# Optimization experiments

Hardware: AMD Instinct MI355X
Metric: run time of the kernel (lower is better)

## Reference

```python
import jax, jax.numpy as jnp
import numpy as np

B, S, H, STEPS = 4096, 169, 64, 24  # batch, input seq (window 168 + covariate row), hidden, rollout steps


def _lstm(xseq, Wih, Whh, bih, bhh, h0, c0):
    """PyTorch-style single-layer LSTM. xseq: [B,T,D] -> ([B,T,H], hT, cT). Gate order i,f,g,o."""
    xg = jnp.einsum('btd,gd->btg', xseq, Wih) + (bih + bhh)  # precompute input proj [B,T,4H]

    def step(carry, xg_t):
        h, c = carry
        g = xg_t + h @ Whh.T
        i, f, gg, o = jnp.split(g, 4, axis=-1)
        c = jax.nn.sigmoid(f) * c + jax.nn.sigmoid(i) * jnp.tanh(gg)
        h = jax.nn.sigmoid(o) * jnp.tanh(c)
        return (h, c), h

    (hT, cT), hs = jax.lax.scan(step, (h0, c0), jnp.swapaxes(xg, 0, 1))
    return jnp.swapaxes(hs, 0, 1), hT, cT


def reference(x, Wih1, Whh1, bih1, bhh1, Wih2, Whh2, bih2, bhh2, fc1_w, fc1_b, fc2_w, fc2_b):
    win, d = x[:, :-1, :], x[:, -1, :]  # [B,168,1], [B,1]
    z = jnp.zeros((x.shape[0], H), x.dtype)

    def outer(win, _):
        h1s, h1, c1 = _lstm(win, Wih1, Whh1, bih1, bhh1, z, z)
        h1s = jax.nn.relu(h1s)
        # lstm2 is seeded with lstm1's final (h, c) state, as in the torch code
        h2s, _, _ = _lstm(h1s, Wih2, Whh2, bih2, bhh2, h1, c1)
        feat = jnp.concatenate([jax.nn.relu(h2s[:, -1, :]), d], axis=1)  # [B,65]
        out = (feat @ fc1_w.T + fc1_b) @ fc2_w.T + fc2_b  # [B,1] (no relu between fc1/fc2)
        win = jnp.concatenate([win[:, 1:, :], out[:, :, None]], axis=1)  # slide window
        return win, out[:, 0]

    _, outs = jax.lax.scan(outer, win, None, length=STEPS)  # outs: [24,B]
    return jnp.swapaxes(outs, 0, 1)  # [B,24]


def setup_inputs() -> dict:
    key = jax.random.key(0)
    ks = jax.random.split(key, 14)
    bnd = 1.0 / np.sqrt(H)

    def u(k, shape):
        return jax.random.uniform(k, shape, jnp.float32, -bnd, bnd)

    return {
        'x': jax.random.normal(ks[0], (B, S, 1), jnp.float32),
        'Wih1': u(ks[1], (4 * H, 1)),
        'Whh1': u(ks[2], (4 * H, H)),
        'bih1': u(ks[3], (4 * H,)),
        'bhh1': u(ks[4], (4 * H,)),
        'Wih2': u(ks[5], (4 * H, H)),
        'Whh2': u(ks[6], (4 * H, H)),
        'bih2': u(ks[7], (4 * H,)),
        'bhh2': u(ks[8], (4 * H,)),
        'fc1_w': u(ks[9], (64, 65)),
        'fc1_b': u(ks[10], (64,)),
        'fc2_w': u(ks[11], (1, 64)),
        'fc2_b': u(ks[12], (1,)),
    }
```

## Files before the change

### kernel.cpp

```cpp
#include <hip/hip_runtime.h>
#include <stdint.h>

#define NB 16
#define WIN 168
#define NSTEPS 24
#define NBLK (4096/NB)
#define NT 512

typedef __attribute__((ext_vector_type(8))) short bf16x8;
typedef __attribute__((ext_vector_type(4))) float f32x4;

#if __has_builtin(__builtin_amdgcn_rcpf)
#define RCPF(x) __builtin_amdgcn_rcpf(x)
#else
#define RCPF(x) (1.0f / (x))
#endif
#if __has_builtin(__builtin_amdgcn_exp2f)
#define EXP2F(x) __builtin_amdgcn_exp2f(x)
#else
#define EXP2F(x) __expf((x) * 0.6931471805599453f)
#endif

__device__ __forceinline__ float sigm(float x){
  return RCPF(1.0f + EXP2F(x * -1.4426950408889634f));
}
__device__ __forceinline__ float sigtanh(float a, float b){
  float A = EXP2F(a * -1.4426950408889634f);
  float B = EXP2F(fabsf(b) * -2.8853900817779268f);
  float t = (1.0f - B) * RCPF((1.0f + A) * (1.0f + B));
  return __builtin_copysignf(t, b);
}

__device__ __forceinline__ uint32_t bf_rn(float f){
  uint32_t u = __builtin_bit_cast(uint32_t, f);
  return (u + 0x7FFFu + ((u >> 16) & 1u)) >> 16;
}
__device__ __forceinline__ float bf_f(uint32_t s){
  return __builtin_bit_cast(float, s << 16);
}
__device__ __forceinline__ void split_t(float f, uint32_t& hi, uint32_t& lo){
  uint32_t u = __builtin_bit_cast(uint32_t, f);
  hi = u >> 16;
  lo = bf_rn(f - bf_f(hi));
}
__device__ __forceinline__ void split_s(float f, short& hi, short& lo){
  uint32_t h = bf_rn(f);
  hi = (short)h;
  lo = (short)bf_rn(f - bf_f(h));
}
__device__ __forceinline__ uint32_t cvtpk2(float a, float b){
  uint32_t r;
  asm("v_cvt_pk_bf16_f32 %0, %1, %2" : "=v"(r) : "v"(a), "v"(b));
  return r;
}
__device__ __forceinline__ float hi_even(uint32_t p){
  return __builtin_bit_cast(float, p << 16);
}
__device__ __forceinline__ float hi_odd(uint32_t p){
  return __builtin_bit_cast(float, p & 0xFFFF0000u);
}
__device__ __forceinline__ f32x4 mfma16(bf16x8 a, bf16x8 b, f32x4 c){
  return __builtin_amdgcn_mfma_f32_16x16x32_bf16(a, b, c, 0, 0, 0);
}

#define FROW 136
#define FBLK 544
#define FB(buf,hl,kt) ((((buf)*2 + (hl))*2 + (kt)) * FBLK)
#define BUF_INTS (2*FBLK)

__global__ __launch_bounds__(NT, 2) void lstm_fused_kernel(
  const float* __restrict__ x,    const float* __restrict__ Wih1, const float* __restrict__ Whh1,
  const float* __restrict__ bih1, const float* __restrict__ bhh1,
  const float* __restrict__ Wih2, const float* __restrict__ Whh2,
  const float* __restrict__ bih2, const float* __restrict__ bhh2,
  const float* __restrict__ fc1w, const float* __restrict__ fc1b,
  const float* __restrict__ fc2w, const float* __restrict__ fc2b,
  float* __restrict__ out, short* __restrict__ hist)
{
  __shared__ __align__(16) short aS[2*2*2*FBLK];
  __shared__ __align__(16) short bS[2*2*2*FBLK];
  __shared__ float win_s[WIN][NB];
  __shared__ float Hlast[NB][68];
  __shared__ float fc1w_s[64*68];
  __shared__ float dval_s[NB];

  const int tid = threadIdx.x;
  const int w   = tid >> 6;
  const int ln  = tid & 63;
  const int q   = ln >> 4;
  const int n   = ln & 15;
  const int bg0 = blockIdx.x * NB;
  const int rdo = q*FROW + n*8;
  const int ro  = q*128 + n*8;
  const int ktw = w >> 2;
  const int wrw = (w&3)*FROW + n*8 + 2*q;
  const int hwo = ktw*512 + (w&3)*128 + n*8 + 2*q;
  short* __restrict__ hblk = hist + (size_t)blockIdx.x * WIN * 2048;

  for (int i = tid; i < WIN*NB; i += NT){ int t = i >> 4, b = i & 15; win_s[t][b] = x[(bg0 + b)*169 + t]; }
  for (int i = tid; i < 64*65; i += NT){ int j = i / 65, k = i % 65; fc1w_s[j*68 + k] = fc1w[i]; }
  if (tid < NB) dval_s[tid] = x[(bg0 + tid)*169 + 168];

  const float fc1b_r = fc1b[ln];
  const float fc2w_r = fc2w[ln];
  const float fc2b_r = fc2b[0];

  auto fc_head = [&](int s){
    float o2[2];
    #pragma unroll
    for (int bi = 0; bi < 2; bi++){
      const int b = 2*w + bi;
      float a1 = fc1b_r;
      #pragma unroll
      for (int k4 = 0; k4 < 16; k4++){
        const float* wp = &fc1w_s[ln*68 + k4*4];
        const float* hp = &Hlast[b][k4*4];
        a1 += wp[0]*hp[0] + wp[1]*hp[1] + wp[2]*hp[2] + wp[3]*hp[3];
      }
      a1 += dval_s[b] * fc1w_s[ln*68 + 64];
      float v = a1 * fc2w_r;
      #pragma unroll
      for (int off = 32; off > 0; off >>= 1) v += __shfl_xor(v, off);
      o2[bi] = v + fc2b_r;
    }
    if (ln == 0){
      #pragma unroll
      for (int bi = 0; bi < 2; bi++){
        const int b = 2*w + bi;
        out[(bg0 + b)*24 + s] = o2[bi];
        win_s[s % WIN][b] = o2[bi];
      }
    }
  };

  bf16x8 A1hi[2][2], A1lo[2][2], Ain1[2];
  bf16x8 A2hi[2][4], A2lo[2][4];
  f32x4 b1c[2], b2c[2];
  #pragma unroll
  for (int tu = 0; tu < 2; tu++){
    const int jA = 64*(n&3) + 8*w + 2*(n>>2) + tu;
    #pragma unroll
    for (int kt = 0; kt < 2; kt++){
      const float* pw = Whh1 + jA*64 + kt*32 + q*8;
      #pragma unroll
      for (int jj = 0; jj < 8; jj++){ short h,l; split_s(pw[jj], h, l); A1hi[tu][kt][jj] = h; A1lo[tu][kt][jj] = l; }
    }
    bf16x8 ain = {0,0,0,0,0,0,0,0};
    if (q == 0){ short wh, wl; split_s(Wih1[jA], wh, wl); ain[0] = wh; ain[1] = wh; ain[2] = wl; }
    Ain1[tu] = ain;
    #pragma unroll
    for (int kt = 0; kt < 4; kt++){
      const float* pw = (kt < 2 ? (Wih2 + jA*64 + kt*32) : (Whh2 + jA*64 + (kt-2)*32)) + q*8;
      #pragma unroll
      for (int jj = 0; jj < 8; jj++){ short h,l; split_s(pw[jj], h, l); A2hi[tu][kt][jj] = h; A2lo[tu][kt][jj] = l; }
    }
    const int U = 8*w + 2*q + tu;
    #pragma unroll
    for (int r = 0; r < 4; r++){
      b1c[tu][r] = bih1[64*r + U] + bhh1[64*r + U];
      b2c[tu][r] = bih2[64*r + U] + bhh2[64*r + U];
    }
  }

  float c1[2], c1sav[2], c2[2];
  bf16x8 hA0, lA0, hA1, lA1, hB0, lB0, hB1, lB1;

  auto loadA = [&](int t){
    const short* Hp = hblk + (size_t)t * 2048;
    hA0 = *(const bf16x8*)&Hp[ro];
    lA0 = *(const bf16x8*)&Hp[1024 + ro];
    hA1 = *(const bf16x8*)&Hp[512 + ro];
    lA1 = *(const bf16x8*)&Hp[1536 + ro];
  };
  auto loadB = [&](int t){
    const short* Hp = hblk + (size_t)t * 2048;
    hB0 = *(const bf16x8*)&Hp[ro];
    lB0 = *(const bf16x8*)&Hp[1024 + ro];
    hB1 = *(const bf16x8*)&Hp[512 + ro];
    lB1 = *(const bf16x8*)&Hp[1536 + ro];
  };

  auto lstm1 = [&](int rb, int wb, int slot, int t, bool first){
    bf16x8 bin = {0,0,0,0,0,0,0,0};
    { float xv = win_s[slot][n];
      uint32_t xp = cvtpk2(xv, xv);
      float rx = xv - hi_even(xp);
      uint32_t xq = cvtpk2(rx, rx);
      if (q == 0){ bin[0] = (short)xp; bin[1] = (short)xq; bin[2] = (short)xp; } }
    f32x4 acc[2];
    if (first){
      #pragma unroll
      for (int tu = 0; tu < 2; tu++) acc[tu] = mfma16(Ain1[tu], bin, b1c[tu]);
    } else {
      bf16x8 Bh0 = *(const bf16x8*)&aS[FB(rb,0,0)+rdo];
      bf16x8 Bl0 = *(const bf16x8*)&aS[FB(rb,1,0)+rdo];
      bf16x8 Bh1 = *(const bf16x8*)&aS[FB(rb,0,1)+rdo];
      bf16x8 Bl1 = *(const bf16x8*)&aS[FB(rb,1,1)+rdo];
      #pragma unroll
      for (int tu = 0; tu < 2; tu++){
        f32x4 a = b1c[tu];
        a = mfma16(A1hi[tu][0], Bh0, a);
        a = mfma16(A1hi[tu][0], Bl0, a);
        a = mfma16(A1lo[tu][0], Bh0, a);
        a = mfma16(A1hi[tu][1], Bh1, a);
        a = mfma16(A1hi[tu][1], Bl1, a);
        a = mfma16(A1lo[tu][1], Bh1, a);
        a = mfma16(Ain1[tu], bin, a);
        acc[tu] = a;
      }
    }
    float hn[2];
    #pragma unroll
    for (int tu = 0; tu < 2; tu++){
      float cn = __builtin_fmaf(sigm(acc[tu][1]), c1[tu], sigtanh(acc[tu][0], acc[tu][2]));
      c1[tu] = cn;
      hn[tu] = sigtanh(acc[tu][3], cn);
    }
    uint32_t p  = cvtpk2(hn[0], hn[1]);
    float r0 = hn[0] - hi_even(p), r1 = hn[1] - hi_odd(p);
    uint32_t ql = cvtpk2(r0, r1);
    *(uint32_t*)&aS[FB(wb,0,ktw)+wrw] = p;
    *(uint32_t*)&aS[FB(wb,1,ktw)+wrw] = ql;
    uint32_t m = (hn[0] > 0.0f ? 0x0000FFFFu : 0u) | (hn[1] > 0.0f ? 0xFFFF0000u : 0u);
    short* Hp = hblk + (size_t)t * 2048;
    *(uint32_t*)&Hp[hwo]        = p  & m;
    *(uint32_t*)&Hp[1024 + hwo] = ql & m;
  };

  auto lstm2 = [&](bf16x8 h0, bf16x8 l0, bf16x8 h1, bf16x8 l1,
                   const short* Sr, int rb, short* Sw, int wb, bool last){
    bf16x8 Sh0 = *(const bf16x8*)&Sr[FB(rb,0,0)+rdo];
    bf16x8 Sl0 = *(const bf16x8*)&Sr[FB(rb,1,0)+rdo];
    bf16x8 Sh1 = *(const bf16x8*)&Sr[FB(rb,0,1)+rdo];
    bf16x8 Sl1 = *(const bf16x8*)&Sr[FB(rb,1,1)+rdo];
    f32x4 acc[2];
    #pragma unroll
    for (int tu = 0; tu < 2; tu++){
      f32x4 a = b2c[tu];
      a = mfma16(A2hi[tu][0], h0, a);
      a = mfma16(A2hi[tu][0], l0, a);
      a = mfma16(A2lo[tu][0], h0, a);
      a = mfma16(A2hi[tu][1], h1, a);
      a = mfma16(A2hi[tu][1], l1, a);
      a = mfma16(A2lo[tu][1], h1, a);
      a = mfma16(A2hi[tu][2], Sh0, a);
      a = mfma16(A2hi[tu][2], Sl0, a);
      a = mfma16(A2lo[tu][2], Sh0, a);
      a = mfma16(A2hi[tu][3], Sh1, a);
      a = mfma16(A2hi[tu][3], Sl1, a);
      a = mfma16(A2lo[tu][3], Sh1, a);
      acc[tu] = a;
    }
    float hn[2];
    #pragma unroll
    for (int tu = 0; tu < 2; tu++){
      float cn = __builtin_fmaf(sigm(acc[tu][1]), c2[tu], sigtanh(acc[tu][0], acc[tu][2]));
      c2[tu] = cn;
      hn[tu] = sigtanh(acc[tu][3], cn);
    }
    if (!last){
      uint32_t p  = cvtpk2(hn[0], hn[1]);
      float r0 = hn[0] - hi_even(p), r1 = hn[1] - hi_odd(p);
      uint32_t ql = cvtpk2(r0, r1);
      *(uint32_t*)&Sw[FB(wb,0,ktw)+wrw] = p;
      *(uint32_t*)&Sw[FB(wb,1,ktw)+wrw] = ql;
    } else {
      const int U0 = 8*w + 2*q;
      Hlast[n][U0]     = fmaxf(hn[0], 0.0f);
      Hlast[n][U0 + 1] = fmaxf(hn[1], 0.0f);
    }
  };

  c1[0] = 0.0f; c1[1] = 0.0f;
  __syncthreads();
  lstm1(0, 1, 0, 0, true);
  for (int t = 1; t < WIN-1; t += 2){
    __syncthreads();
    lstm1(1, 0, t, t, false);
    __syncthreads();
    lstm1(0, 1, t+1, t+1, false);
  }
  __syncthreads();
  lstm1(1, 0, WIN-1, WIN-1, false);
  c1sav[0] = c1[0]; c1sav[1] = c1[1];

  for (int sg = 1; sg < NSTEPS; sg++){
    c2[0] = c1sav[0]; c2[1] = c1sav[1];
    c1[0] = 0.0f;     c1[1] = 0.0f;
    loadA(0); loadB(1);
    int slot = sg;
    __syncthreads();
    lstm1(0, 1, slot, 0, true); slot++;
    lstm2(hA0, lA0, hA1, lA1, aS, 0, bS, 1, false);
    for (int t = 1; t < WIN-1; t += 2){
      __syncthreads();
      loadA(t + 1);
      lstm1(1, 0, slot, t, false); slot++; if (slot == WIN) slot = 0;
      lstm2(hB0, lB0, hB1, lB1, bS, 1, bS, 0, false);
      __syncthreads();
      loadB(t + 2);
      lstm1(0, 1, slot, t+1, false); slot++; if (slot == WIN) slot = 0;
      lstm2(hA0, lA0, hA1, lA1, bS, 0, bS, 1, false);
    }
    __syncthreads();
    lstm2(hB0, lB0, hB1, lB1, bS, 1, bS, 0, true);
    __syncthreads();
    fc_head(sg - 1);
    __syncthreads();
    lstm1(1, 0, slot, WIN-1, false);
    c1sav[0] = c1[0]; c1sav[1] = c1[1];
  }

  {
    c2[0] = c1sav[0]; c2[1] = c1sav[1];
    loadA(0); loadB(1);
    __syncthreads();
    lstm2(hA0, lA0, hA1, lA1, aS, 0, bS, 1, false);
    for (int t = 1; t < WIN-1; t += 2){
      __syncthreads();
      loadA(t + 1);
      lstm2(hB0, lB0, hB1, lB1, bS, 1, bS, 0, false);
      __syncthreads();
      loadB(t + 2);
      lstm2(hA0, lA0, hA1, lA1, bS, 0, bS, 1, false);
    }
    __syncthreads();
    lstm2(hB0, lB0, hB1, lB1, bS, 1, bS, 0, true);
    __syncthreads();
    fc_head(NSTEPS - 1);
  }
}

__global__ __launch_bounds__(256, 1) void lstm_fallback_kernel(
  const float* __restrict__ x,    const float* __restrict__ Wih1, const float* __restrict__ Whh1,
  const float* __restrict__ bih1, const float* __restrict__ bhh1,
  const float* __restrict__ Wih2, const float* __restrict__ Whh2,
  const float* __restrict__ bih2, const float* __restrict__ bhh2,
  const float* __restrict__ fc1w, const float* __restrict__ fc1b,
  const float* __restrict__ fc2w, const float* __restrict__ fc2b,
  float* __restrict__ out)
{
  __shared__ __align__(16) short aS[2*2*2*FBLK];
  __shared__ __align__(16) short r1f[2*2*2*FBLK];
  __shared__ __align__(16) short rlf[2*2*2*FBLK];
  __shared__ float win_s[WIN][NB];
  __shared__ float Hlast[NB][68];
  __shared__ float fc1w_s[64*68];
  __shared__ float dval_s[NB];

  const int tid = threadIdx.x;
  const int wv  = tid >> 6;
  const int ln  = tid & 63;
  const int q   = ln >> 4;
  const int n   = ln & 15;
  const int bg0 = blockIdx.x * NB;
  const int u0  = 16*wv + 4*q;
  const int kt_  = u0 >> 5;
  const int q2_  = (u0 >> 3) & 3;
  const int jj0_ = u0 & 7;
  const int rdo  = q*FROW + n*8;
  const int wro  = q2_*FROW + n*8 + jj0_;

  for (int i = tid; i < WIN*NB; i += 256){ int t = i >> 4, b = i & 15; win_s[t][b] = x[(bg0 + b)*169 + t]; }
  for (int i = tid; i < 64*65; i += 256){ int j = i / 65, k = i % 65; fc1w_s[j*68 + k] = fc1w[i]; }
  if (tid < NB) dval_s[tid] = x[(bg0 + tid)*169 + 168];

  const float fc1b_r = fc1b[ln];
  const float fc2w_r = fc2w[ln];
  const float fc2b_r = fc2b[0];

  bf16x8 A1hi[4][2], A1lo[4][2], Ain1[4];
  bf16x8 A2hi[4][4], A2lo[4][4];
  f32x4 b1c[4], b2c[4];
  #pragma unroll
  for (int e = 0; e < 4; e++){
    const int ja = 64*e + 16*wv + n;
    #pragma unroll
    for (int kt = 0; kt < 2; kt++){
      const float* pw = Whh1 + ja*64 + kt*32 + q*8;
      #pragma unroll
      for (int jj = 0; jj < 8; jj++){ short h,l; split_s(pw[jj], h, l); A1hi[e][kt][jj] = h; A1lo[e][kt][jj] = l; }
    }
    #pragma unroll
    for (int kt = 0; kt < 4; kt++){
      const float* pw = (kt < 2 ? (Wih2 + ja*64 + kt*32) : (Whh2 + ja*64 + (kt-2)*32)) + q*8;
      #pragma unroll
      for (int jj = 0; jj < 8; jj++){ short h,l; split_s(pw[jj], h, l); A2hi[e][kt][jj] = h; A2lo[e][kt][jj] = l; }
    }
    bf16x8 ain = {0,0,0,0,0,0,0,0};
    if (q == 0){ short wh, wl; split_s(Wih1[ja], wh, wl); ain[0] = wh; ain[1] = wh; ain[2] = wl; }
    Ain1[e] = ain;
    const int jc = 64*e + u0;
    #pragma unroll
    for (int r = 0; r < 4; r++){
      b1c[e][r] = bih1[jc+r] + bhh1[jc+r];
      b2c[e][r] = bih2[jc+r] + bhh2[jc+r];
    }
  }

  float c1[4], c2[4], c1r[4];

  auto lstm1_step = [&](short* S, float* cst, int rb, int wb, int slot, bool relu_out){
    bf16x8 Bh0 = *(const bf16x8*)&S[FB(rb,0,0)+rdo];
    bf16x8 Bl0 = *(const bf16x8*)&S[FB(rb,1,0)+rdo];
    bf16x8 Bh1 = *(const bf16x8*)&S[FB(rb,0,1)+rdo];
    bf16x8 Bl1 = *(const bf16x8*)&S[FB(rb,1,1)+rdo];
    bf16x8 bin = {0,0,0,0,0,0,0,0};
    { float xv = win_s[slot][n]; uint32_t xh, xl; split_t(xv, xh, xl);
      if (q == 0){ bin[0] = (short)xh; bin[1] = (short)xl; bin[2] = (short)xh; } }
    f32x4 acc[4];
    #pragma unroll
    for (int e = 0; e < 4; e++){
      f32x4 a = b1c[e];
      a = mfma16(A1hi[e][0], Bh0, a);
      a = mfma16(A1hi[e][0], Bl0, a);
      a = mfma16(A1lo[e][0], Bh0, a);
      a = mfma16(A1hi[e][1], Bh1, a);
      a = mfma16(A1hi[e][1], Bl1, a);
      a = mfma16(A1lo[e][1], Bh1, a);
      a = mfma16(Ain1[e], bin, a);
      acc[e] = a;
    }
    float hn[4];
    #pragma unroll
    for (int r = 0; r < 4; r++){
      float cn = __builtin_fmaf(sigm(acc[1][r]), cst[r], sigtanh(acc[0][r], acc[2][r]));
      cst[r] = cn;
      hn[r] = sigtanh(acc[3][r], cn);
    }
    uint32_t ph[4], pl[4];
    #pragma unroll
    for (int r = 0; r < 4; r++) split_t(hn[r], ph[r], pl[r]);
    *(uint2*)&S[FB(wb,0,kt_)+wro] = make_uint2(ph[0] | (ph[1]<<16), ph[2] | (ph[3]<<16));
    *(uint2*)&S[FB(wb,1,kt_)+wro] = make_uint2(pl[0] | (pl[1]<<16), pl[2] | (pl[3]<<16));
    if (relu_out){
      uint32_t sh[4], sl[4];
      #pragma unroll
      for (int r = 0; r < 4; r++){ bool pos = hn[r] > 0.0f; sh[r] = pos ? ph[r] : 0u; sl[r] = pos ? pl[r] : 0u; }
      *(uint2*)&rlf[FB(rb,0,kt_)+wro] = make_uint2(sh[0] | (sh[1]<<16), sh[2] | (sh[3]<<16));
      *(uint2*)&rlf[FB(rb,1,kt_)+wro] = make_uint2(sl[0] | (sl[1]<<16), sl[2] | (sl[3]<<16));
    }
  };

  auto lstm2_core = [&](bf16x8 L1h0, bf16x8 L1l0, bf16x8 L1h1, bf16x8 L1l1,
                        int rbuf, int wbuf, bool last){
    bf16x8 L2h0 = *(const bf16x8*)&aS[FB(rbuf,0,0)+rdo];
    bf16x8 L2l0 = *(const bf16x8*)&aS[FB(rbuf,1,0)+rdo];
    bf16x8 L2h1 = *(const bf16x8*)&aS[FB(rbuf,0,1)+rdo];
    bf16x8 L2l1 = *(const bf16x8*)&aS[FB(rbuf,1,1)+rdo];
    f32x4 acc[4];
    #pragma unroll
    for (int e = 0; e < 4; e++){
      f32x4 a = b2c[e];
      a = mfma16(A2hi[e][0], L1h0, a);
      a = mfma16(A2hi[e][0], L1l0, a);
      a = mfma16(A2lo[e][0], L1h0, a);
      a = mfma16(A2hi[e][1], L1h1, a);
      a = mfma16(A2hi[e][1], L1l1, a);
      a = mfma16(A2lo[e][1], L1h1, a);
      a = mfma16(A2hi[e][2], L2h0, a);
      a = mfma16(A2hi[e][2], L2l0, a);
      a = mfma16(A2lo[e][2], L2h0, a);
      a = mfma16(A2hi[e][3], L2h1, a);
      a = mfma16(A2hi[e][3], L2l1, a);
      a = mfma16(A2lo[e][3], L2h1, a);
      acc[e] = a;
    }
    float hn[4];
    #pragma unroll
    for (int r = 0; r < 4; r++){
      float cn = __builtin_fmaf(sigm(acc[1][r]), c2[r], sigtanh(acc[0][r], acc[2][r]));
      c2[r] = cn;
      hn[r] = sigtanh(acc[3][r], cn);
    }
    if (!last){
      uint32_t ph[4], pl[4];
      #pragma unroll
      for (int r = 0; r < 4; r++) split_t(hn[r], ph[r], pl[r]);
      *(uint2*)&aS[FB(wbuf,0,kt_)+wro] = make_uint2(ph[0] | (ph[1]<<16), ph[2] | (ph[3]<<16));
      *(uint2*)&aS[FB(wbuf,1,kt_)+wro] = make_uint2(pl[0] | (pl[1]<<16), pl[2] | (pl[3]<<16));
    } else {
      #pragma unroll
      for (int r = 0; r < 4; r++) Hlast[n][u0 + r] = fmaxf(hn[r], 0.0f);
    }
  };

  for (int s = 0; s < NSTEPS; s++){
    { int* p = (int*)&aS[0];
      for (int i = tid; i < BUF_INTS; i += 256) p[i] = 0; }
    #pragma unroll
    for (int r = 0; r < 4; r++) c1[r] = 0.0f;
    int slot = s;
    for (int t = 0; t < WIN; t++){
      __syncthreads();
      lstm1_step(aS, c1, t & 1, (t & 1) ^ 1, slot, false);
      slot++; if (slot == WIN) slot = 0;
    }
    #pragma unroll
    for (int r = 0; r < 4; r++){ c2[r] = c1[r]; c1r[r] = 0.0f; }
    { int* p = (int*)&r1f[0];
      for (int i = tid; i < BUF_INTS; i += 256) p[i] = 0; }
    slot = s;
    __syncthreads();
    lstm1_step(r1f, c1r, 0, 1, slot, true);
    slot++;
    for (int i = 1; i < WIN; i++){
      __syncthreads();
      const int rb = i & 1, wb = rb ^ 1;
      lstm1_step(r1f, c1r, rb, wb, slot, true);
      bf16x8 L1h0 = *(const bf16x8*)&rlf[FB(wb,0,0)+rdo];
      bf16x8 L1l0 = *(const bf16x8*)&rlf[FB(wb,1,0)+rdo];
      bf16x8 L1h1 = *(const bf16x8*)&rlf[FB(wb,0,1)+rdo];
      bf16x8 L1l1 = *(const bf16x8*)&rlf[FB(wb,1,1)+rdo];
      lstm2_core(L1h0, L1l0, L1h1, L1l1, wb, rb, false);
      slot++; if (slot == WIN) slot = 0;
    }
    __syncthreads();
    {
      const int rb = (WIN - 1) & 1;
      bf16x8 L1h0 = *(const bf16x8*)&rlf[FB(rb,0,0)+rdo];
      bf16x8 L1l0 = *(const bf16x8*)&rlf[FB(rb,1,0)+rdo];
      bf16x8 L1h1 = *(const bf16x8*)&rlf[FB(rb,0,1)+rdo];
      bf16x8 L1l1 = *(const bf16x8*)&rlf[FB(rb,1,1)+rdo];
      lstm2_core(L1h0, L1l0, L1h1, L1l1, rb, 0, true);
    }
    __syncthreads();
    {
      float o4[4];
      #pragma unroll
      for (int bi = 0; bi < 4; bi++){
        const int b = 4*wv + bi;
        float a1 = fc1b_r;
        #pragma unroll
        for (int k4 = 0; k4 < 16; k4++){
          const float* wp = &fc1w_s[ln*68 + k4*4];
          const float* hp = &Hlast[b][k4*4];
          a1 += wp[0]*hp[0] + wp[1]*hp[1] + wp[2]*hp[2] + wp[3]*hp[3];
        }
        a1 += dval_s[b] * fc1w_s[ln*68 + 64];
        float v = a1 * fc2w_r;
        #pragma unroll
        for (int off = 32; off > 0; off >>= 1) v += __shfl_xor(v, off);
        o4[bi] = v + fc2b_r;
      }
      if (ln == 0){
        #pragma unroll
        for (int bi = 0; bi < 4; bi++){
          const int b = 4*wv + bi;
          out[(bg0 + b)*24 + s] = o4[bi];
          win_s[s % WIN][b] = o4[bi];
        }
      }
    }
  }
}

extern "C" void kernel_launch(void* const* d_in, const int* in_sizes, int n_in,
                              void* d_out, int out_size, void* d_ws, size_t ws_size,
                              hipStream_t stream) {
  (void)in_sizes; (void)n_in; (void)out_size;
  const size_t need = (size_t)NBLK * WIN * 2048 * sizeof(short);
  if (ws_size >= need){
    lstm_fused_kernel<<<dim3(NBLK), dim3(NT), 0, stream>>>(
        (const float*)d_in[0], (const float*)d_in[1], (const float*)d_in[2],
        (const float*)d_in[3], (const float*)d_in[4], (const float*)d_in[5],
        (const float*)d_in[6], (const float*)d_in[7], (const float*)d_in[8],
        (const float*)d_in[9], (const float*)d_in[10], (const float*)d_in[11],
        (const float*)d_in[12], (float*)d_out, (short*)d_ws);
  } else {
    lstm_fallback_kernel<<<dim3(NBLK), dim3(256), 0, stream>>>(
        (const float*)d_in[0], (const float*)d_in[1], (const float*)d_in[2],
        (const float*)d_in[3], (const float*)d_in[4], (const float*)d_in[5],
        (const float*)d_in[6], (const float*)d_in[7], (const float*)d_in[8],
        (const float*)d_in[9], (const float*)d_in[10], (const float*)d_in[11],
        (const float*)d_in[12], (float*)d_out);
  }
}
```

Before: 5.010 ms.

## Split LSTM layers across specialized wave groups with doubled block size

Doubles the block to 1024 threads. The first 8 waves run only the layer-1 recurrence and the other 8 run only the layer-2 recurrence, so both layers advance concurrently in separate waves. The two groups stay in lockstep through matched barrier counts, and the layer-1 final cell state is handed to layer 2 through a new shared-memory array. The aim is a shorter serial chain per timestep and fewer live weight registers per wave. The cost is a more fragile barrier protocol and a launch-bounds occupancy hint of 4 blocks of 1024 threads, which may squeeze the per-thread register budget and cause spills.

```diff
diff --git a/kernel.cpp b/kernel.cpp
--- a/kernel.cpp
+++ b/kernel.cpp
@@ -5,7 +5,7 @@
 #define WIN 168
 #define NSTEPS 24
 #define NBLK (4096/NB)
-#define NT 512
+#define NT 1024
 
 typedef __attribute__((ext_vector_type(8))) short bf16x8;
 typedef __attribute__((ext_vector_type(4))) float f32x4;
@@ -68,7 +68,7 @@
 #define FB(buf,hl,kt) ((((buf)*2 + (hl))*2 + (kt)) * FBLK)
 #define BUF_INTS (2*FBLK)
 
-__global__ __launch_bounds__(NT, 2) void lstm_fused_kernel(
+__global__ __launch_bounds__(NT, 4) void lstm_fused_kernel(
   const float* __restrict__ x,    const float* __restrict__ Wih1, const float* __restrict__ Whh1,
   const float* __restrict__ bih1, const float* __restrict__ bhh1,
   const float* __restrict__ Wih2, const float* __restrict__ Whh2,
@@ -79,13 +79,16 @@
 {
   __shared__ __align__(16) short aS[2*2*2*FBLK];
   __shared__ __align__(16) short bS[2*2*2*FBLK];
+  __shared__ float cS[64][16];
   __shared__ float win_s[WIN][NB];
   __shared__ float Hlast[NB][68];
   __shared__ float fc1w_s[64*68];
   __shared__ float dval_s[NB];
 
   const int tid = threadIdx.x;
-  const int w   = tid >> 6;
+  const int w16 = tid >> 6;
+  const int w   = w16 & 7;
+  const bool isA = (w16 < 8);
   const int ln  = tid & 63;
   const int q   = ln >> 4;
   const int n   = ln & 15;
@@ -106,228 +109,261 @@
   const float fc2b_r = fc2b[0];
 
   auto fc_head = [&](int s){
-    float o2[2];
-    #pragma unroll
-    for (int bi = 0; bi < 2; bi++){
-      const int b = 2*w + bi;
-      float a1 = fc1b_r;
-      #pragma unroll
-      for (int k4 = 0; k4 < 16; k4++){
-        const float* wp = &fc1w_s[ln*68 + k4*4];
-        const float* hp = &Hlast[b][k4*4];
-        a1 += wp[0]*hp[0] + wp[1]*hp[1] + wp[2]*hp[2] + wp[3]*hp[3];
-      }
-      a1 += dval_s[b] * fc1w_s[ln*68 + 64];
-      float v = a1 * fc2w_r;
-      #pragma unroll
-      for (int off = 32; off > 0; off >>= 1) v += __shfl_xor(v, off);
-      o2[bi] = v + fc2b_r;
-    }
+    const int b = w16;
+    float a1 = fc1b_r;
+    #pragma unroll
+    for (int k4 = 0; k4 < 16; k4++){
+      const float* wp = &fc1w_s[ln*68 + k4*4];
+      const float* hp = &Hlast[b][k4*4];
+      a1 += wp[0]*hp[0] + wp[1]*hp[1] + wp[2]*hp[2] + wp[3]*hp[3];
+    }
+    a1 += dval_s[b] * fc1w_s[ln*68 + 64];
+    float v = a1 * fc2w_r;
+    #pragma unroll
+    for (int off = 32; off > 0; off >>= 1) v += __shfl_xor(v, off);
     if (ln == 0){
-      #pragma unroll
-      for (int bi = 0; bi < 2; bi++){
-        const int b = 2*w + bi;
-        out[(bg0 + b)*24 + s] = o2[bi];
-        win_s[s % WIN][b] = o2[bi];
-      }
+      float o = v + fc2b_r;
+      out[(bg0 + b)*24 + s] = o;
+      win_s[s % WIN][b] = o;
     }
   };
 
-  bf16x8 A1hi[2][2], A1lo[2][2], Ain1[2];
-  bf16x8 A2hi[2][4], A2lo[2][4];
-  f32x4 b1c[2], b2c[2];
-  #pragma unroll
-  for (int tu = 0; tu < 2; tu++){
-    const int jA = 64*(n&3) + 8*w + 2*(n>>2) + tu;
-    #pragma unroll
-    for (int kt = 0; kt < 2; kt++){
-      const float* pw = Whh1 + jA*64 + kt*32 + q*8;
-      #pragma unroll
-      for (int jj = 0; jj < 8; jj++){ short h,l; split_s(pw[jj], h, l); A1hi[tu][kt][jj] = h; A1lo[tu][kt][jj] = l; }
-    }
-    bf16x8 ain = {0,0,0,0,0,0,0,0};
-    if (q == 0){ short wh, wl; split_s(Wih1[jA], wh, wl); ain[0] = wh; ain[1] = wh; ain[2] = wl; }
-    Ain1[tu] = ain;
-    #pragma unroll
-    for (int kt = 0; kt < 4; kt++){
-      const float* pw = (kt < 2 ? (Wih2 + jA*64 + kt*32) : (Whh2 + jA*64 + (kt-2)*32)) + q*8;
-      #pragma unroll
-      for (int jj = 0; jj < 8; jj++){ short h,l; split_s(pw[jj], h, l); A2hi[tu][kt][jj] = h; A2lo[tu][kt][jj] = l; }
-    }
-    const int U = 8*w + 2*q + tu;
-    #pragma unroll
-    for (int r = 0; r < 4; r++){
-      b1c[tu][r] = bih1[64*r + U] + bhh1[64*r + U];
-      b2c[tu][r] = bih2[64*r + U] + bhh2[64*r + U];
-    }
-  }
-
-  float c1[2], c1sav[2], c2[2];
-  bf16x8 hA0, lA0, hA1, lA1, hB0, lB0, hB1, lB1;
-
-  auto loadA = [&](int t){
-    const short* Hp = hblk + (size_t)t * 2048;
-    hA0 = *(const bf16x8*)&Hp[ro];
-    lA0 = *(const bf16x8*)&Hp[1024 + ro];
-    hA1 = *(const bf16x8*)&Hp[512 + ro];
-    lA1 = *(const bf16x8*)&Hp[1536 + ro];
-  };
-  auto loadB = [&](int t){
-    const short* Hp = hblk + (size_t)t * 2048;
-    hB0 = *(const bf16x8*)&Hp[ro];
-    lB0 = *(const bf16x8*)&Hp[1024 + ro];
-    hB1 = *(const bf16x8*)&Hp[512 + ro];
-    lB1 = *(const bf16x8*)&Hp[1536 + ro];
-  };
-
-  auto lstm1 = [&](int rb, int wb, int slot, int t, bool first){
-    bf16x8 bin = {0,0,0,0,0,0,0,0};
-    { float xv = win_s[slot][n];
-      uint32_t xp = cvtpk2(xv, xv);
-      float rx = xv - hi_even(xp);
-      uint32_t xq = cvtpk2(rx, rx);
-      if (q == 0){ bin[0] = (short)xp; bin[1] = (short)xq; bin[2] = (short)xp; } }
-    f32x4 acc[2];
-    if (first){
-      #pragma unroll
-      for (int tu = 0; tu < 2; tu++) acc[tu] = mfma16(Ain1[tu], bin, b1c[tu]);
-    } else {
-      bf16x8 Bh0 = *(const bf16x8*)&aS[FB(rb,0,0)+rdo];
-      bf16x8 Bl0 = *(const bf16x8*)&aS[FB(rb,1,0)+rdo];
-      bf16x8 Bh1 = *(const bf16x8*)&aS[FB(rb,0,1)+rdo];
-      bf16x8 Bl1 = *(const bf16x8*)&aS[FB(rb,1,1)+rdo];
+  if (isA){
+    bf16x8 A1hi[2][2], A1lo[2][2], Ain1[2];
+    f32x4 b1c[2];
+    #pragma unroll
+    for (int tu = 0; tu < 2; tu++){
+      const int jA = 64*(n&3) + 8*w + 2*(n>>2) + tu;
+      #pragma unroll
+      for (int kt = 0; kt < 2; kt++){
+        const float* pw = Whh1 + jA*64 + kt*32 + q*8;
+        #pragma unroll
+        for (int jj = 0; jj < 8; jj++){ short h,l; split_s(pw[jj], h, l); A1hi[tu][kt][jj] = h; A1lo[tu][kt][jj] = l; }
+      }
+      bf16x8 ain = {0,0,0,0,0,0,0,0};
+      if (q == 0){ short wh, wl; split_s(Wih1[jA], wh, wl); ain[0] = wh; ain[1] = wh; ain[2] = wl; }
+      Ain1[tu] = ain;
+      const int U = 8*w + 2*q + tu;
+      #pragma unroll
+      for (int r = 0; r < 4; r++) b1c[tu][r] = bih1[64*r + U] + bhh1[64*r + U];
+    }
+    float c1[2];
+
+    auto lstm1 = [&](int rb, int wb, int slot, int t, bool first){
+      bf16x8 bin = {0,0,0,0,0,0,0,0};
+      { float xv = win_s[slot][n];
+        uint32_t xp = cvtpk2(xv, xv);
+        float rx = xv - hi_even(xp);
+        uint32_t xq = cvtpk2(rx, rx);
+        if (q == 0){ bin[0] = (short)xp; bin[1] = (short)xq; bin[2] = (short)xp; } }
+      f32x4 acc[2];
+      if (first){
+        #pragma unroll
+        for (int tu = 0; tu < 2; tu++) acc[tu] = mfma16(Ain1[tu], bin, b1c[tu]);
+      } else {
+        bf16x8 Bh0 = *(const bf16x8*)&aS[FB(rb,0,0)+rdo];
+        bf16x8 Bl0 = *(const bf16x8*)&aS[FB(rb,1,0)+rdo];
+        bf16x8 Bh1 = *(const bf16x8*)&aS[FB(rb,0,1)+rdo];
+        bf16x8 Bl1 = *(const bf16x8*)&aS[FB(rb,1,1)+rdo];
+        #pragma unroll
+        for (int tu = 0; tu < 2; tu++){
+          f32x4 a = b1c[tu];
+          a = mfma16(A1hi[tu][0], Bh0, a);
+          a = mfma16(A1hi[tu][0], Bl0, a);
+          a = mfma16(A1lo[tu][0], Bh0, a);
+          a = mfma16(A1hi[tu][1], Bh1, a);
+          a = mfma16(A1hi[tu][1], Bl1, a);
+          a = mfma16(A1lo[tu][1], Bh1, a);
+          a = mfma16(Ain1[tu], bin, a);
+          acc[tu] = a;
+        }
+      }
+      float hn[2];
       #pragma unroll
       for (int tu = 0; tu < 2; tu++){
-        f32x4 a = b1c[tu];
-        a = mfma16(A1hi[tu][0], Bh0, a);
-        a = mfma16(A1hi[tu][0], Bl0, a);
-        a = mfma16(A1lo[tu][0], Bh0, a);
-        a = mfma16(A1hi[tu][1], Bh1, a);
-        a = mfma16(A1hi[tu][1], Bl1, a);
-        a = mfma16(A1lo[tu][1], Bh1, a);
-        a = mfma16(Ain1[tu], bin, a);
-        acc[tu] = a;
-      }
-    }
-    float hn[2];
-    #pragma unroll
-    for (int tu = 0; tu < 2; tu++){
-      float cn = __builtin_fmaf(sigm(acc[tu][1]), c1[tu], sigtanh(acc[tu][0], acc[tu][2]));
-      c1[tu] = cn;
-      hn[tu] = sigtanh(acc[tu][3], cn);
-    }
-    uint32_t p  = cvtpk2(hn[0], hn[1]);
-    float r0 = hn[0] - hi_even(p), r1 = hn[1] - hi_odd(p);
-    uint32_t ql = cvtpk2(r0, r1);
-    *(uint32_t*)&aS[FB(wb,0,ktw)+wrw] = p;
-    *(uint32_t*)&aS[FB(wb,1,ktw)+wrw] = ql;
-    uint32_t m = (hn[0] > 0.0f ? 0x0000FFFFu : 0u) | (hn[1] > 0.0f ? 0xFFFF0000u : 0u);
-    short* Hp = hblk + (size_t)t * 2048;
-    *(uint32_t*)&Hp[hwo]        = p  & m;
-    *(uint32_t*)&Hp[1024 + hwo] = ql & m;
-  };
-
-  auto lstm2 = [&](bf16x8 h0, bf16x8 l0, bf16x8 h1, bf16x8 l1,
-                   const short* Sr, int rb, short* Sw, int wb, bool last){
-    bf16x8 Sh0 = *(const bf16x8*)&Sr[FB(rb,0,0)+rdo];
-    bf16x8 Sl0 = *(const bf16x8*)&Sr[FB(rb,1,0)+rdo];
-    bf16x8 Sh1 = *(const bf16x8*)&Sr[FB(rb,0,1)+rdo];
-    bf16x8 Sl1 = *(const bf16x8*)&Sr[FB(rb,1,1)+rdo];
-    f32x4 acc[2];
-    #pragma unroll
-    for (int tu = 0; tu < 2; tu++){
-      f32x4 a = b2c[tu];
-      a = mfma16(A2hi[tu][0], h0, a);
-      a = mfma16(A2hi[tu][0], l0, a);
-      a = mfma16(A2lo[tu][0], h0, a);
-      a = mfma16(A2hi[tu][1], h1, a);
-      a = mfma16(A2hi[tu][1], l1, a);
-      a = mfma16(A2lo[tu][1], h1, a);
-      a = mfma16(A2hi[tu][2], Sh0, a);
-      a = mfma16(A2hi[tu][2], Sl0, a);
-      a = mfma16(A2lo[tu][2], Sh0, a);
-      a = mfma16(A2hi[tu][3], Sh1, a);
-      a = mfma16(A2hi[tu][3], Sl1, a);
-      a = mfma16(A2lo[tu][3], Sh1, a);
-      acc[tu] = a;
-    }
-    float hn[2];
-    #pragma unroll
-    for (int tu = 0; tu < 2; tu++){
-      float cn = __builtin_fmaf(sigm(acc[tu][1]), c2[tu], sigtanh(acc[tu][0], acc[tu][2]));
-      c2[tu] = cn;
-      hn[tu] = sigtanh(acc[tu][3], cn);
-    }
-    if (!last){
+        float cn = __builtin_fmaf(sigm(acc[tu][1]), c1[tu], sigtanh(acc[tu][0], acc[tu][2]));
+        c1[tu] = cn;
+        hn[tu] = sigtanh(acc[tu][3], cn);
+      }
       uint32_t p  = cvtpk2(hn[0], hn[1]);
       float r0 = hn[0] - hi_even(p), r1 = hn[1] - hi_odd(p);
       uint32_t ql = cvtpk2(r0, r1);
-      *(uint32_t*)&Sw[FB(wb,0,ktw)+wrw] = p;
-      *(uint32_t*)&Sw[FB(wb,1,ktw)+wrw] = ql;
-    } else {
-      const int U0 = 8*w + 2*q;
-      Hlast[n][U0]     = fmaxf(hn[0], 0.0f);
-      Hlast[n][U0 + 1] = fmaxf(hn[1], 0.0f);
-    }
-  };
-
-  c1[0] = 0.0f; c1[1] = 0.0f;
-  __syncthreads();
-  lstm1(0, 1, 0, 0, true);
-  for (int t = 1; t < WIN-1; t += 2){
+      *(uint32_t*)&aS[FB(wb,0,ktw)+wrw] = p;
+      *(uint32_t*)&aS[FB(wb,1,ktw)+wrw] = ql;
+      uint32_t m = (hn[0] > 0.0f ? 0x0000FFFFu : 0u) | (hn[1] > 0.0f ? 0xFFFF0000u : 0u);
+      short* Hp = hblk + (size_t)t * 2048;
+      *(uint32_t*)&Hp[hwo]        = p  & m;
+      *(uint32_t*)&Hp[1024 + hwo] = ql & m;
+    };
+
+    c1[0] = 0.0f; c1[1] = 0.0f;
     __syncthreads();
-    lstm1(1, 0, t, t, false);
+    lstm1(0, 1, 0, 0, true);
+    for (int t = 1; t < WIN-1; t += 2){
+      __syncthreads();
+      lstm1(1, 0, t, t, false);
+      __syncthreads();
+      lstm1(0, 1, t+1, t+1, false);
+    }
     __syncthreads();
-    lstm1(0, 1, t+1, t+1, false);
-  }
-  __syncthreads();
-  lstm1(1, 0, WIN-1, WIN-1, false);
-  c1sav[0] = c1[0]; c1sav[1] = c1[1];
-
-  for (int sg = 1; sg < NSTEPS; sg++){
-    c2[0] = c1sav[0]; c2[1] = c1sav[1];
-    c1[0] = 0.0f;     c1[1] = 0.0f;
-    loadA(0); loadB(1);
-    int slot = sg;
-    __syncthreads();
-    lstm1(0, 1, slot, 0, true); slot++;
-    lstm2(hA0, lA0, hA1, lA1, aS, 0, bS, 1, false);
-    for (int t = 1; t < WIN-1; t += 2){
-      __syncthreads();
-      loadA(t + 1);
-      lstm1(1, 0, slot, t, false); slot++; if (slot == WIN) slot = 0;
-      lstm2(hB0, lB0, hB1, lB1, bS, 1, bS, 0, false);
-      __syncthreads();
-      loadB(t + 2);
-      lstm1(0, 1, slot, t+1, false); slot++; if (slot == WIN) slot = 0;
-      lstm2(hA0, lA0, hA1, lA1, bS, 0, bS, 1, false);
-    }
-    __syncthreads();
-    lstm2(hB0, lB0, hB1, lB1, bS, 1, bS, 0, true);
-    __syncthreads();
-    fc_head(sg - 1);
-    __syncthreads();
-    lstm1(1, 0, slot, WIN-1, false);
-    c1sav[0] = c1[0]; c1sav[1] = c1[1];
-  }
-
-  {
-    c2[0] = c1sav[0]; c2[1] = c1sav[1];
-    loadA(0); loadB(1);
-    __syncthreads();
-    lstm2(hA0, lA0, hA1, lA1, aS, 0, bS, 1, false);
-    for (int t = 1; t < WIN-1; t += 2){
-      __syncthreads();
-      loadA(t + 1);
-      lstm2(hB0, lB0, hB1, lB1, bS, 1, bS, 0, false);
-      __syncthreads();
-      loadB(t + 2);
-      lstm2(hA0, lA0, hA1, lA1, bS, 0, bS, 1, false);
-    }
-    __syncthreads();
-    lstm2(hB0, lB0, hB1, lB1, bS, 1, bS, 0, true);
-    __syncthreads();
+    lstm1(1, 0, WIN-1, WIN-1, false);
+    #pragma unroll
+    for (int tu = 0; tu < 2; tu++) cS[8*w + 2*q + tu][n] = c1[tu];
+
+    for (int sg = 1; sg < NSTEPS; sg++){
+      c1[0] = 0.0f; c1[1] = 0.0f;
+      int slot = sg;
+      __syncthreads();
+      lstm1(0, 1, slot, 0, true);
+      slot++;
+      for (int t = 1; t < WIN-1; t += 2){
+        __syncthreads();
+        lstm1(1, 0, slot, t, false);
+        slot++; if (slot == WIN) slot = 0;
+        __syncthreads();
+        lstm1(0, 1, slot, t+1, false);
+        slot++; if (slot == WIN) slot = 0;
+      }
+      __syncthreads();
+      __syncthreads();
+      fc_head(sg - 1);
+      __syncthreads();
+      lstm1(1, 0, slot, WIN-1, false);
+      #pragma unroll
+      for (int tu = 0; tu < 2; tu++) cS[8*w + 2*q + tu][n] = c1[tu];
+    }
+
+    for (int i = 0; i < WIN + 1; i++) __syncthreads();
     fc_head(NSTEPS - 1);
+
+  } else {
+    bf16x8 A2hi[2][4], A2lo[2][4];
+    f32x4 b2c[2];
+    #pragma unroll
+    for (int tu = 0; tu < 2; tu++){
+      const int jA = 64*(n&3) + 8*w + 2*(n>>2) + tu;
+      #pragma unroll
+      for (int kt = 0; kt < 4; kt++){
+        const float* pw = (kt < 2 ? (Wih2 + jA*64 + kt*32) : (Whh2 + jA*64 + (kt-2)*32)) + q*8;
+        #pragma unroll
+        for (int jj = 0; jj < 8; jj++){ short h,l; split_s(pw[jj], h, l); A2hi[tu][kt][jj] = h; A2lo[tu][kt][jj] = l; }
+      }
+      const int U = 8*w + 2*q + tu;
+      #pragma unroll
+      for (int r = 0; r < 4; r++) b2c[tu][r] = bih2[64*r + U] + bhh2[64*r + U];
+    }
+    float c2[2];
+    bf16x8 ch0, cl0, ch1, cl1, nh0, nl0, nh1, nl1;
+
+    auto loadc = [&](int t){
+      const short* Hp = hblk + (size_t)t * 2048;
+      ch0 = *(const bf16x8*)&Hp[ro];
+      cl0 = *(const bf16x8*)&Hp[1024 + ro];
+      ch1 = *(const bf16x8*)&Hp[512 + ro];
+      cl1 = *(const bf16x8*)&Hp[1536 + ro];
+    };
+    auto loadn = [&](int t){
+      const short* Hp = hblk + (size_t)t * 2048;
+      nh0 = *(const bf16x8*)&Hp[ro];
+      nl0 = *(const bf16x8*)&Hp[1024 + ro];
+      nh1 = *(const bf16x8*)&Hp[512 + ro];
+      nl1 = *(const bf16x8*)&Hp[1536 + ro];
+    };
+    auto shift = [&](){ ch0 = nh0; cl0 = nl0; ch1 = nh1; cl1 = nl1; };
+
+    auto lstm2 = [&](const short* Sr, int rb, short* Sw, int wb, bool last){
+      bf16x8 Sh0 = *(const bf16x8*)&Sr[FB(rb,0,0)+rdo];
+      bf16x8 Sl0 = *(const bf16x8*)&Sr[FB(rb,1,0)+rdo];
+      bf16x8 Sh1 = *(const bf16x8*)&Sr[FB(rb,0,1)+rdo];
+      bf16x8 Sl1 = *(const bf16x8*)&Sr[FB(rb,1,1)+rdo];
+      f32x4 acc[2];
+      #pragma unroll
+      for (int tu = 0; tu < 2; tu++){
+        f32x4 a = b2c[tu];
+        a = mfma16(A2hi[tu][0], ch0, a);
+        a = mfma16(A2hi[tu][0], cl0, a);
+        a = mfma16(A2lo[tu][0], ch0, a);
+        a = mfma16(A2hi[tu][1], ch1, a);
+        a = mfma16(A2hi[tu][1], cl1, a);
+        a = mfma16(A2lo[tu][1], ch1, a);
+        a = mfma16(A2hi[tu][2], Sh0, a);
+        a = mfma16(A2hi[tu][2], Sl0, a);
+        a = mfma16(A2lo[tu][2], Sh0, a);
+        a = mfma16(A2hi[tu][3], Sh1, a);
+        a = mfma16(A2hi[tu][3], Sl1, a);
+        a = mfma16(A2lo[tu][3], Sh1, a);
+        acc[tu] = a;
+      }
+      float hn[2];
+      #pragma unroll
+      for (int tu = 0; tu < 2; tu++){
+        float cn = __builtin_fmaf(sigm(acc[tu][1]), c2[tu], sigtanh(acc[tu][0], acc[tu][2]));
+        c2[tu] = cn;
+        hn[tu] = sigtanh(acc[tu][3], cn);
+      }
+      if (!last){
+        uint32_t p  = cvtpk2(hn[0], hn[1]);
+        float r0 = hn[0] - hi_even(p), r1 = hn[1] - hi_odd(p);
+        uint32_t ql = cvtpk2(r0, r1);
+        *(uint32_t*)&Sw[FB(wb,0,ktw)+wrw] = p;
+        *(uint32_t*)&Sw[FB(wb,1,ktw)+wrw] = ql;
+      } else {
+        const int U0 = 8*w + 2*q;
+        Hlast[n][U0]     = fmaxf(hn[0], 0.0f);
+        Hlast[n][U0 + 1] = fmaxf(hn[1], 0.0f);
+      }
+    };
+
+    for (int i = 0; i < WIN; i++) __syncthreads();
+
+    for (int sg = 1; sg < NSTEPS; sg++){
+      loadc(0);
+      loadn(1);
+      __syncthreads();
+      #pragma unroll
+      for (int tu = 0; tu < 2; tu++) c2[tu] = cS[8*w + 2*q + tu][n];
+      lstm2(aS, 0, bS, 1, false);
+      shift();
+      for (int t = 1; t < WIN-1; t += 2){
+        __syncthreads();
+        loadn(t + 1);
+        lstm2(bS, 1, bS, 0, false);
+        shift();
+        __syncthreads();
+        loadn(t + 2);
+        lstm2(bS, 0, bS, 1, false);
+        shift();
+      }
+      __syncthreads();
+      lstm2(bS, 1, bS, 0, true);
+      __syncthreads();
+      fc_head(sg - 1);
+      __syncthreads();
+    }
+
+    {
+      loadc(0);
+      loadn(1);
+      __syncthreads();
+      #pragma unroll
+      for (int tu = 0; tu < 2; tu++) c2[tu] = cS[8*w + 2*q + tu][n];
+      lstm2(aS, 0, bS, 1, false);
+      shift();
+      for (int t = 1; t < WIN-1; t += 2){
+        __syncthreads();
+        loadn(t + 1);
+        lstm2(bS, 1, bS, 0, false);
+        shift();
+        __syncthreads();
+        loadn(t + 2);
+        lstm2(bS, 0, bS, 1, false);
+        shift();
+      }
+      __syncthreads();
+      lstm2(bS, 1, bS, 0, true);
+      __syncthreads();
+      fc_head(NSTEPS - 1);
+    }
   }
 }
 
```

Result: no change. 4.957 ms (-1.1%).
